# Performance work log

Measured on AMD Instinct MI355X. Metric: run time of the kernel, lower is better.

## Reference

```python
import jax, jax.numpy as jnp
import numpy as np

EPS = 1e-6
NEG_SLOPE = 0.2


def _basis(J):
    # J: [B,N,E,3] -> R: [B,N,E,3(k: U,V,J rows),3(xyz comp)]
    nJ = J / (jnp.linalg.norm(J, axis=-1, keepdims=True) + EPS)
    sub = nJ[..., :2]
    u_z = -(sub[..., 0] ** 2 + sub[..., 1] ** 2) / (nJ[..., 2] + EPS)
    U = jnp.concatenate([sub, u_z[..., None]], axis=-1)
    U = U / (jnp.linalg.norm(U, axis=-1, keepdims=True) + EPS)
    V = jnp.cross(U, nJ)
    return jnp.stack([U, V, nJ], axis=-2)


def _complex_linear(X, J, A, Bw, Cw):
    R = _basis(J)                                   # [B,N,E,3,3], R[...,k,i]
    RtX = jnp.einsum('bneki,bnek->bnei', R, X)      # (R^T X)_i = sum_k R[k,i] X_k
    # rrtx(i, s) has component k equal to R[...,k,i] * s
    a_term = R[..., 0] * RtX[..., 0:1] + R[..., 1] * RtX[..., 1:2]
    b_term = R[..., 1] * RtX[..., 0:1] - R[..., 0] * RtX[..., 1:2]
    c_term = R[..., 2] * RtX[..., 2:3]
    Y = (jnp.einsum('fe,bnei->bnfi', A, a_term)
         + jnp.einsum('fe,bnei->bnfi', Bw, b_term)
         + jnp.einsum('fe,bnei->bnfi', Cw, c_term))
    return Y                                        # [B,N,F,3]


def _vn_leaky_relu(x, W, negative_slope):
    # x: [B,F,3,N]; W: [F,F] torch Linear weight (out,in)
    d = jnp.einsum('gf,bfin->bgin', W, x)
    dot = jnp.sum(x * d, axis=2, keepdims=True)
    d_norm_sq = jnp.sum(d * d, axis=2, keepdims=True)
    neg_branch = x - (dot / (d_norm_sq + EPS)) * d
    lin = jnp.where(dot >= 0, x, neg_branch)
    return negative_slope * x + (1.0 - negative_slope) * lin


def setup_inputs() -> dict:
    key = jax.random.key(0)
    kX, kJ, kA, kB, kC, kW = jax.random.split(key, 6)
    B, N, E, F = 16, 1024, 256, 256
    X = jax.random.normal(kX, (B, N, E, 3), dtype=jnp.float32)
    J = jax.random.normal(kJ, (B, N, E, 3), dtype=jnp.float32)
    A = jax.random.normal(kA, (F, E), dtype=jnp.float32)
    Bw = jax.random.normal(kB, (F, E), dtype=jnp.float32)
    Cw = jax.random.normal(kC, (F, E), dtype=jnp.float32)
    W = jax.random.normal(kW, (F, F), dtype=jnp.float32) * (1.0 / np.sqrt(F))
    return {"X": X, "J": J, "A": A, "Bw": Bw, "Cw": Cw, "W": W, "device": 0}


def reference(X, J, A, Bw, Cw, W, device):
    Y = _complex_linear(X, J, A, Bw, Cw)            # [B,N,F,3]
    x = jnp.transpose(Y, (0, 2, 3, 1))              # [B,F,3,N]
    return _vn_leaky_relu(x, W, NEG_SLOPE)
```

## Files before the change

### kernel.cpp

```cpp
#include <hip/hip_runtime.h>

typedef __attribute__((ext_vector_type(8))) _Float16 half8;
typedef __attribute__((ext_vector_type(4))) _Float16 half4v;
typedef __attribute__((ext_vector_type(4))) float f32x4;
typedef float f32x4u __attribute__((ext_vector_type(4), aligned(4)));
typedef float f32x2u __attribute__((ext_vector_type(2), aligned(4)));

#define EPSF 1e-6f

__device__ __forceinline__ void glds16(const void* g, void* l) {
    __builtin_amdgcn_global_load_lds(
        (const __attribute__((address_space(1))) unsigned*)g,
        (__attribute__((address_space(3))) unsigned*)l, 16, 0, 0);
}
__device__ __forceinline__ unsigned short h2u(_Float16 h) {
    union { _Float16 h; unsigned short u; } c; c.h = h; return c.u;
}

__global__ __launch_bounds__(256) void prep_kernel(
    const float* __restrict__ A, const float* __restrict__ Bw,
    const float* __restrict__ Cw, const float* __restrict__ W,
    _Float16* __restrict__ Mh, _Float16* __restrict__ Wh)
{
    int f = blockIdx.x, e = threadIdx.x;
    Mh[f * 768 + e]       = (_Float16)A[f * 256 + e];
    Mh[f * 768 + 256 + e] = (_Float16)Bw[f * 256 + e];
    Mh[f * 768 + 512 + e] = (_Float16)Cw[f * 256 + e];
    Wh[f * 256 + e]       = (_Float16)W[f * 256 + e];
}

__global__ __launch_bounds__(512, 4) void fused_kernel(
    const float* __restrict__ X, const float* __restrict__ Jp,
    const _Float16* __restrict__ Mh, const _Float16* __restrict__ Wh,
    float* __restrict__ out)
{
    extern __shared__ char lds[];
    const int T_OFF = 49152;
    int tid = threadIdx.x;
    int b  = blockIdx.x >> 5;
    int n0 = (blockIdx.x & 31) * 32;

    int l = tid & 63, lr = l & 15, lq = l >> 4;
    int w = tid >> 6, wc = w & 1, wf = w >> 1;
    int nl = tid >> 4, ep = tid & 15;

    size_t pb0 = ((size_t)((b * 1024 + n0 + nl) * 256) + 2 * ep) * 3;

    auto loadXJ = [&](int eb, float* xs, float* js) {
        size_t pb = pb0 + (size_t)eb * 96;
        f32x4u xa = *(const f32x4u*)(X + pb);
        f32x2u xb = *(const f32x2u*)(X + pb + 4);
        f32x4u ja = *(const f32x4u*)(Jp + pb);
        f32x2u jb = *(const f32x2u*)(Jp + pb + 4);
        xs[0]=xa[0]; xs[1]=xa[1]; xs[2]=xa[2]; xs[3]=xa[3]; xs[4]=xb[0]; xs[5]=xb[1];
        js[0]=ja[0]; js[1]=ja[1]; js[2]=ja[2]; js[3]=ja[3]; js[4]=jb[0]; js[5]=jb[1];
    };

    auto stageA = [&](int eb) {
        #pragma unroll
        for (int h = 0; h < 6; ++h) {
            int m = h * 512 + tid;
            int t = m >> 10, fr = (m >> 2) & 255, slot = m & 3;
            size_t go = ((size_t)fr * 768 + t * 256 + eb * 32
                         + ((slot ^ ((fr >> 1) & 3)) * 8)) * 2;
            glds16((const char*)Mh + go, lds + m * 16);
        }
    };

    auto computeT = [&](const float* xs, const float* js) {
        unsigned short hv[2][9];
        #pragma unroll
        for (int p = 0; p < 2; ++p) {
            float x0 = xs[3*p], x1 = xs[3*p+1], x2 = xs[3*p+2];
            float j0 = js[3*p], j1 = js[3*p+1], j2 = js[3*p+2];
            float jj  = j0*j0 + j1*j1 + j2*j2;
            float rn  = __builtin_amdgcn_rcpf(__builtin_amdgcn_sqrtf(jj) + EPSF);
            float nj0 = j0*rn, nj1 = j1*rn, nj2 = j2*rn;
            float s2  = nj0*nj0 + nj1*nj1;
            float uz  = -s2 * __builtin_amdgcn_rcpf(nj2 + EPSF);
            float ru  = __builtin_amdgcn_rcpf(__builtin_amdgcn_sqrtf(s2 + uz*uz) + EPSF);
            float u0 = nj0*ru, u1 = nj1*ru, u2 = uz*ru;
            float v0 = u1*nj2 - u2*nj1;
            float v1 = u2*nj0 - u0*nj2;
            float v2 = u0*nj1 - u1*nj0;
            float r0 = u0*x0 + v0*x1 + nj0*x2;
            float r1 = u1*x0 + v1*x1 + nj1*x2;
            float r2 = u2*x0 + v2*x1 + nj2*x2;
            hv[p][0] = h2u((_Float16)(u0*r0 + u1*r1));
            hv[p][1] = h2u((_Float16)(v0*r0 + v1*r1));
            hv[p][2] = h2u((_Float16)(nj0*r0 + nj1*r1));
            hv[p][3] = h2u((_Float16)(u1*r0 - u0*r1));
            hv[p][4] = h2u((_Float16)(v1*r0 - v0*r1));
            hv[p][5] = h2u((_Float16)(nj1*r0 - nj0*r1));
            hv[p][6] = h2u((_Float16)(u2*r2));
            hv[p][7] = h2u((_Float16)(v2*r2));
            hv[p][8] = h2u((_Float16)(nj2*r2));
        }
        #pragma unroll
        for (int s = 0; s < 9; ++s) {
            int t = s / 3, i = s % 3;
            unsigned pk = (unsigned)hv[0][s] | ((unsigned)hv[1][s] << 16);
            *(unsigned*)(lds + T_OFF + (t * 96 + i * 32 + nl) * 80 + ep * 4) = pk;
        }
    };

    f32x4 acc[3][4] = {};
    float xs[6], js[6];
    loadXJ(0, xs, js);

    for (int eb = 0; eb < 8; ++eb) {
        __syncthreads();
        stageA(eb);
        computeT(xs, js);
        __syncthreads();
        if (eb < 7) loadXJ(eb + 1, xs, js);

        #pragma unroll
        for (int t = 0; t < 3; ++t) {
            half8 af[4], bf[3];
            #pragma unroll
            for (int mi = 0; mi < 4; ++mi) {
                int f = wf * 64 + mi * 16 + lr;
                af[mi] = *(const half8*)(lds + t * 16384 + f * 64
                                         + ((lq ^ ((f >> 1) & 3)) * 16));
            }
            #pragma unroll
            for (int bi = 0; bi < 3; ++bi) {
                int cr = wc * 48 + bi * 16 + lr;
                bf[bi] = *(const half8*)(lds + T_OFF + (t * 96 + cr) * 80 + lq * 16);
            }
            #pragma unroll
            for (int bi = 0; bi < 3; ++bi)
                #pragma unroll
                for (int mi = 0; mi < 4; ++mi)
                    acc[bi][mi] = __builtin_amdgcn_mfma_f32_16x16x32_f16(af[mi], bf[bi], acc[bi][mi], 0, 0, 0);
        }
    }

    __syncthreads();
    #pragma unroll
    for (int bi = 0; bi < 3; ++bi) {
        int c = wc * 48 + bi * 16 + lr;
        #pragma unroll
        for (int mi = 0; mi < 4; ++mi) {
            int fb2 = (wf * 64 + mi * 16 + lq * 4) * 2;
            f32x4 v = acc[bi][mi];
            half4v p;
            p.x = (_Float16)v[0]; p.y = (_Float16)v[1];
            p.z = (_Float16)v[2]; p.w = (_Float16)v[3];
            *(half4v*)(lds + c * 512 + (fb2 ^ ((c & 7) << 4))) = p;
        }
    }

    int nh = w & 1, gw = w >> 1;
    half8 wreg[2][4];
    #pragma unroll
    for (int gf = 0; gf < 4; ++gf) {
        int g = gw * 64 + gf * 16 + lr;
        wreg[0][gf] = *(const half8*)(Wh + (size_t)g * 256 + lq * 8);
    }
    __syncthreads();

    f32x4 acc2[3][4] = {};
    #pragma unroll
    for (int kt = 0; kt < 8; ++kt) {
        if (kt < 7) {
            #pragma unroll
            for (int gf = 0; gf < 4; ++gf) {
                int g = gw * 64 + gf * 16 + lr;
                wreg[(kt + 1) & 1][gf] =
                    *(const half8*)(Wh + (size_t)g * 256 + (kt + 1) * 32 + lq * 8);
            }
        }
        half8 yf[3];
        #pragma unroll
        for (int ci = 0; ci < 3; ++ci) {
            int c = ci * 32 + nh * 16 + lr;
            yf[ci] = *(const half8*)(lds + c * 512
                                     + ((kt * 64 + lq * 16) ^ ((c & 7) << 4)));
        }
        #pragma unroll
        for (int ci = 0; ci < 3; ++ci)
            #pragma unroll
            for (int gf = 0; gf < 4; ++gf)
                acc2[ci][gf] = __builtin_amdgcn_mfma_f32_16x16x32_f16(
                    yf[ci], wreg[kt & 1][gf], acc2[ci][gf], 0, 0, 0);
    }

    #pragma unroll
    for (int gf = 0; gf < 4; ++gf) {
        int g = gw * 64 + gf * 16 + lr;
        f32x4 o[3];
        #pragma unroll
        for (int r = 0; r < 4; ++r) {
            float xv[3];
            #pragma unroll
            for (int ci = 0; ci < 3; ++ci) {
                int c = ci * 32 + nh * 16 + lq * 4 + r;
                xv[ci] = (float)*(const _Float16*)(lds + c * 512
                                 + ((g * 2) ^ ((c & 7) << 4)));
            }
            float d0 = acc2[0][gf][r], d1 = acc2[1][gf][r], d2 = acc2[2][gf][r];
            float dot = xv[0] * d0 + xv[1] * d1 + xv[2] * d2;
            float dn  = d0 * d0 + d1 * d1 + d2 * d2;
            float sc  = dot / (dn + EPSF);
            bool pos  = dot >= 0.0f;
            float l0 = pos ? xv[0] : fmaf(-sc, d0, xv[0]);
            float l1 = pos ? xv[1] : fmaf(-sc, d1, xv[1]);
            float l2 = pos ? xv[2] : fmaf(-sc, d2, xv[2]);
            o[0][r] = fmaf(0.8f, l0, 0.2f * xv[0]);
            o[1][r] = fmaf(0.8f, l1, 0.2f * xv[1]);
            o[2][r] = fmaf(0.8f, l2, 0.2f * xv[2]);
        }
        int nb = n0 + nh * 16 + lq * 4;
        #pragma unroll
        for (int i = 0; i < 3; ++i)
            *(f32x4*)(out + ((size_t)(b * 256 + g) * 3 + i) * 1024 + nb) = o[i];
    }
}

extern "C" void kernel_launch(void* const* d_in, const int* in_sizes, int n_in,
                              void* d_out, int out_size, void* d_ws, size_t ws_size,
                              hipStream_t stream)
{
    const float* X  = (const float*)d_in[0];
    const float* J  = (const float*)d_in[1];
    const float* A  = (const float*)d_in[2];
    const float* Bw = (const float*)d_in[3];
    const float* Cw = (const float*)d_in[4];
    const float* W  = (const float*)d_in[5];
    float* out = (float*)d_out;

    char* ws = (char*)d_ws;
    _Float16* Mh = (_Float16*)ws;
    _Float16* Wh = (_Float16*)(ws + 393216);

    (void)hipFuncSetAttribute((const void*)fused_kernel,
                              hipFuncAttributeMaxDynamicSharedMemorySize, 72192);

    hipLaunchKernelGGL(prep_kernel,  dim3(256), dim3(256), 0, stream,
                       A, Bw, Cw, W, Mh, Wh);
    hipLaunchKernelGGL(fused_kernel, dim3(512), dim3(512), 72192, stream,
                       X, J, Mh, Wh, out);
}
```

Measured before the change: 58.56 us.

## Double-buffer weight staging and double the per-block point tile with 1024-thread blocks

Each block now covers 64 points instead of 32, using 1024 threads and 256 blocks, so each staged fp16 weight chunk is reused across twice as many points. Weight chunks are double-buffered in LDS so the next chunk's global-to-LDS copy overlaps the current MFMA work. `__syncthreads` is replaced with raw barriers, explicit waitcnt and sched_barrier fences to control ordering. The second GEMM and the epilogue are retiled for the larger block. The cost is about 141 KB of LDS per block, so one block per CU and a single wave of 256 blocks. The hand-written waits cover only LDS counters, so the ordering of the async global-to-LDS copies is fragile.

```diff
diff --git a/kernel.cpp b/kernel.cpp
--- a/kernel.cpp
+++ b/kernel.cpp
@@ -29,23 +29,34 @@
     Wh[f * 256 + e]       = (_Float16)W[f * 256 + e];
 }
 
-__global__ __launch_bounds__(512, 4) void fused_kernel(
+__global__ __launch_bounds__(1024, 2) void fused_kernel(
     const float* __restrict__ X, const float* __restrict__ Jp,
     const _Float16* __restrict__ Mh, const _Float16* __restrict__ Wh,
     float* __restrict__ out)
 {
     extern __shared__ char lds[];
-    const int T_OFF = 49152;
+    const int T_BASE = 98304;
     int tid = threadIdx.x;
-    int b  = blockIdx.x >> 5;
-    int n0 = (blockIdx.x & 31) * 32;
+    int b  = blockIdx.x >> 4;
+    int n0 = (blockIdx.x & 15) * 64;
 
     int l = tid & 63, lr = l & 15, lq = l >> 4;
-    int w = tid >> 6, wc = w & 1, wf = w >> 1;
+    int w = tid >> 6;
+    int wf = w & 3, wc = w >> 2;
     int nl = tid >> 4, ep = tid & 15;
 
+    auto stageEB = [&](int p, int eb) {
+        #pragma unroll
+        for (int h = 0; h < 3; ++h) {
+            int m = h * 1024 + tid;
+            int t = m >> 10, fr = (m >> 2) & 255, slot = m & 3;
+            size_t go = ((size_t)fr * 768 + t * 256 + eb * 32
+                         + ((slot ^ ((fr >> 1) & 3)) * 8)) * 2;
+            glds16((const char*)Mh + go, lds + p * 49152 + m * 16);
+        }
+    };
+
     size_t pb0 = ((size_t)((b * 1024 + n0 + nl) * 256) + 2 * ep) * 3;
-
     auto loadXJ = [&](int eb, float* xs, float* js) {
         size_t pb = pb0 + (size_t)eb * 96;
         f32x4u xa = *(const f32x4u*)(X + pb);
@@ -54,17 +65,6 @@
         f32x2u jb = *(const f32x2u*)(Jp + pb + 4);
         xs[0]=xa[0]; xs[1]=xa[1]; xs[2]=xa[2]; xs[3]=xa[3]; xs[4]=xb[0]; xs[5]=xb[1];
         js[0]=ja[0]; js[1]=ja[1]; js[2]=ja[2]; js[3]=ja[3]; js[4]=jb[0]; js[5]=jb[1];
-    };
-
-    auto stageA = [&](int eb) {
-        #pragma unroll
-        for (int h = 0; h < 6; ++h) {
-            int m = h * 512 + tid;
-            int t = m >> 10, fr = (m >> 2) & 255, slot = m & 3;
-            size_t go = ((size_t)fr * 768 + t * 256 + eb * 32
-                         + ((slot ^ ((fr >> 1) & 3)) * 8)) * 2;
-            glds16((const char*)Mh + go, lds + m * 16);
-        }
     };
 
     auto computeT = [&](const float* xs, const float* js) {
@@ -100,20 +100,34 @@
         for (int s = 0; s < 9; ++s) {
             int t = s / 3, i = s % 3;
             unsigned pk = (unsigned)hv[0][s] | ((unsigned)hv[1][s] << 16);
-            *(unsigned*)(lds + T_OFF + (t * 96 + i * 32 + nl) * 80 + ep * 4) = pk;
+            *(unsigned*)(lds + T_BASE + (t * 192 + i * 64 + nl) * 80 + ep * 4) = pk;
         }
     };
 
     f32x4 acc[3][4] = {};
     float xs[6], js[6];
+
+    stageEB(0, 0);
+    __builtin_amdgcn_sched_barrier(0);
     loadXJ(0, xs, js);
+    __builtin_amdgcn_sched_barrier(0);
 
     for (int eb = 0; eb < 8; ++eb) {
-        __syncthreads();
-        stageA(eb);
+        int cur = eb & 1;
+        __builtin_amdgcn_s_barrier();
+        if (eb < 7) {
+            stageEB(cur ^ 1, eb + 1);
+            __builtin_amdgcn_sched_barrier(0);
+        }
         computeT(xs, js);
-        __syncthreads();
-        if (eb < 7) loadXJ(eb + 1, xs, js);
+        asm volatile("s_waitcnt lgkmcnt(0)" ::: "memory");
+        __builtin_amdgcn_sched_barrier(0);
+        __builtin_amdgcn_s_barrier();
+        __builtin_amdgcn_sched_barrier(0);
+        if (eb < 7) {
+            loadXJ(eb + 1, xs, js);
+            __builtin_amdgcn_sched_barrier(0);
+        }
 
         #pragma unroll
         for (int t = 0; t < 3; ++t) {
@@ -121,23 +135,24 @@
             #pragma unroll
             for (int mi = 0; mi < 4; ++mi) {
                 int f = wf * 64 + mi * 16 + lr;
-                af[mi] = *(const half8*)(lds + t * 16384 + f * 64
+                af[mi] = *(const half8*)(lds + cur * 49152 + t * 16384 + f * 64
                                          + ((lq ^ ((f >> 1) & 3)) * 16));
             }
             #pragma unroll
             for (int bi = 0; bi < 3; ++bi) {
                 int cr = wc * 48 + bi * 16 + lr;
-                bf[bi] = *(const half8*)(lds + T_OFF + (t * 96 + cr) * 80 + lq * 16);
+                bf[bi] = *(const half8*)(lds + T_BASE + (t * 192 + cr) * 80 + lq * 16);
             }
             #pragma unroll
             for (int bi = 0; bi < 3; ++bi)
                 #pragma unroll
                 for (int mi = 0; mi < 4; ++mi)
-                    acc[bi][mi] = __builtin_amdgcn_mfma_f32_16x16x32_f16(af[mi], bf[bi], acc[bi][mi], 0, 0, 0);
-        }
-    }
-
-    __syncthreads();
+                    acc[bi][mi] = __builtin_amdgcn_mfma_f32_16x16x32_f16(
+                        af[mi], bf[bi], acc[bi][mi], 0, 0, 0);
+        }
+    }
+
+    __builtin_amdgcn_s_barrier();
     #pragma unroll
     for (int bi = 0; bi < 3; ++bi) {
         int c = wc * 48 + bi * 16 + lr;
@@ -153,70 +168,74 @@
     }
 
     int nh = w & 1, gw = w >> 1;
-    half8 wreg[2][4];
-    #pragma unroll
-    for (int gf = 0; gf < 4; ++gf) {
-        int g = gw * 64 + gf * 16 + lr;
+    half8 wreg[2][2];
+    #pragma unroll
+    for (int gf = 0; gf < 2; ++gf) {
+        int g = gw * 32 + gf * 16 + lr;
         wreg[0][gf] = *(const half8*)(Wh + (size_t)g * 256 + lq * 8);
     }
-    __syncthreads();
-
-    f32x4 acc2[3][4] = {};
+    asm volatile("s_waitcnt lgkmcnt(0)" ::: "memory");
+    __builtin_amdgcn_sched_barrier(0);
+    __builtin_amdgcn_s_barrier();
+    __builtin_amdgcn_sched_barrier(0);
+
+    f32x4 acc2[3][2][2] = {};
     #pragma unroll
     for (int kt = 0; kt < 8; ++kt) {
         if (kt < 7) {
             #pragma unroll
-            for (int gf = 0; gf < 4; ++gf) {
-                int g = gw * 64 + gf * 16 + lr;
+            for (int gf = 0; gf < 2; ++gf) {
+                int g = gw * 32 + gf * 16 + lr;
                 wreg[(kt + 1) & 1][gf] =
                     *(const half8*)(Wh + (size_t)g * 256 + (kt + 1) * 32 + lq * 8);
             }
         }
-        half8 yf[3];
-        #pragma unroll
-        for (int ci = 0; ci < 3; ++ci) {
-            int c = ci * 32 + nh * 16 + lr;
-            yf[ci] = *(const half8*)(lds + c * 512
-                                     + ((kt * 64 + lq * 16) ^ ((c & 7) << 4)));
-        }
         #pragma unroll
         for (int ci = 0; ci < 3; ++ci)
             #pragma unroll
-            for (int gf = 0; gf < 4; ++gf)
-                acc2[ci][gf] = __builtin_amdgcn_mfma_f32_16x16x32_f16(
-                    yf[ci], wreg[kt & 1][gf], acc2[ci][gf], 0, 0, 0);
-    }
-
-    #pragma unroll
-    for (int gf = 0; gf < 4; ++gf) {
-        int g = gw * 64 + gf * 16 + lr;
-        f32x4 o[3];
-        #pragma unroll
-        for (int r = 0; r < 4; ++r) {
-            float xv[3];
-            #pragma unroll
-            for (int ci = 0; ci < 3; ++ci) {
-                int c = ci * 32 + nh * 16 + lq * 4 + r;
-                xv[ci] = (float)*(const _Float16*)(lds + c * 512
-                                 + ((g * 2) ^ ((c & 7) << 4)));
-            }
-            float d0 = acc2[0][gf][r], d1 = acc2[1][gf][r], d2 = acc2[2][gf][r];
-            float dot = xv[0] * d0 + xv[1] * d1 + xv[2] * d2;
-            float dn  = d0 * d0 + d1 * d1 + d2 * d2;
-            float sc  = dot / (dn + EPSF);
-            bool pos  = dot >= 0.0f;
-            float l0 = pos ? xv[0] : fmaf(-sc, d0, xv[0]);
-            float l1 = pos ? xv[1] : fmaf(-sc, d1, xv[1]);
-            float l2 = pos ? xv[2] : fmaf(-sc, d2, xv[2]);
-            o[0][r] = fmaf(0.8f, l0, 0.2f * xv[0]);
-            o[1][r] = fmaf(0.8f, l1, 0.2f * xv[1]);
-            o[2][r] = fmaf(0.8f, l2, 0.2f * xv[2]);
-        }
-        int nb = n0 + nh * 16 + lq * 4;
-        #pragma unroll
-        for (int i = 0; i < 3; ++i)
-            *(f32x4*)(out + ((size_t)(b * 256 + g) * 3 + i) * 1024 + nb) = o[i];
-    }
+            for (int nc = 0; nc < 2; ++nc) {
+                int c = ci * 64 + nh * 32 + nc * 16 + lr;
+                half8 yf = *(const half8*)(lds + c * 512
+                             + ((kt * 64 + lq * 16) ^ ((c & 7) << 4)));
+                #pragma unroll
+                for (int gf = 0; gf < 2; ++gf)
+                    acc2[ci][nc][gf] = __builtin_amdgcn_mfma_f32_16x16x32_f16(
+                        yf, wreg[kt & 1][gf], acc2[ci][nc][gf], 0, 0, 0);
+            }
+    }
+
+    #pragma unroll
+    for (int nc = 0; nc < 2; ++nc)
+        #pragma unroll
+        for (int gf = 0; gf < 2; ++gf) {
+            int g = gw * 32 + gf * 16 + lr;
+            f32x4 o[3];
+            #pragma unroll
+            for (int r = 0; r < 4; ++r) {
+                float xv[3];
+                #pragma unroll
+                for (int ci = 0; ci < 3; ++ci) {
+                    int c = ci * 64 + nh * 32 + nc * 16 + lq * 4 + r;
+                    xv[ci] = (float)*(const _Float16*)(lds + c * 512
+                                     + ((g * 2) ^ ((c & 7) << 4)));
+                }
+                float d0 = acc2[0][nc][gf][r], d1 = acc2[1][nc][gf][r], d2 = acc2[2][nc][gf][r];
+                float dot = xv[0] * d0 + xv[1] * d1 + xv[2] * d2;
+                float dn  = d0 * d0 + d1 * d1 + d2 * d2;
+                float sc  = dot / (dn + EPSF);
+                bool pos  = dot >= 0.0f;
+                float l0 = pos ? xv[0] : fmaf(-sc, d0, xv[0]);
+                float l1 = pos ? xv[1] : fmaf(-sc, d1, xv[1]);
+                float l2 = pos ? xv[2] : fmaf(-sc, d2, xv[2]);
+                o[0][r] = fmaf(0.8f, l0, 0.2f * xv[0]);
+                o[1][r] = fmaf(0.8f, l1, 0.2f * xv[1]);
+                o[2][r] = fmaf(0.8f, l2, 0.2f * xv[2]);
+            }
+            int nb = n0 + nh * 32 + nc * 16 + lq * 4;
+            #pragma unroll
+            for (int i = 0; i < 3; ++i)
+                *(f32x4*)(out + ((size_t)(b * 256 + g) * 3 + i) * 1024 + nb) = o[i];
+        }
 }
 
 extern "C" void kernel_launch(void* const* d_in, const int* in_sizes, int n_in,
@@ -236,10 +255,10 @@
     _Float16* Wh = (_Float16*)(ws + 393216);
 
     (void)hipFuncSetAttribute((const void*)fused_kernel,
-                              hipFuncAttributeMaxDynamicSharedMemorySize, 72192);
-
-    hipLaunchKernelGGL(prep_kernel,  dim3(256), dim3(256), 0, stream,
+                              hipFuncAttributeMaxDynamicSharedMemorySize, 144384);
+
+    hipLaunchKernelGGL(prep_kernel,  dim3(256), dim3(256),  0, stream,
                        A, Bw, Cw, W, Mh, Wh);
-    hipLaunchKernelGGL(fused_kernel, dim3(512), dim3(512), 72192, stream,
+    hipLaunchKernelGGL(fused_kernel, dim3(256), dim3(1024), 144384, stream,
                        X, J, Mh, Wh, out);
 }
```

Result: faster. 54.83 us (-6.4%).

## Double-buffer per-term A-weight tiles and shrink LDS footprint

Applied to the files above, without the earlier changes.

Replaces staging all three weight slices per E-block with a two-slot ring buffer that stages one term's slice at a time, prefetching the next while MFMAs consume the current one. The T tile row stride drops from 80 to 72 bytes and LDS use falls from about 72 KB to about 53 KB, with launch bounds lowered from 4 to 3 blocks per CU. The register prefetch of X/J for the next block is removed, so those global loads now sit on the critical path before computeT. A barrier is added after every term step, which raises sync count.

```diff
diff --git a/kernel.cpp b/kernel.cpp
--- a/kernel.cpp
+++ b/kernel.cpp
@@ -29,45 +29,44 @@
     Wh[f * 256 + e]       = (_Float16)W[f * 256 + e];
 }
 
-__global__ __launch_bounds__(512, 4) void fused_kernel(
+__global__ __launch_bounds__(512, 3)
+void fused_kernel(
     const float* __restrict__ X, const float* __restrict__ Jp,
     const _Float16* __restrict__ Mh, const _Float16* __restrict__ Wh,
     float* __restrict__ out)
 {
     extern __shared__ char lds[];
-    const int T_OFF = 49152;
+    const int T_BASE = 32768;
     int tid = threadIdx.x;
     int b  = blockIdx.x >> 5;
     int n0 = (blockIdx.x & 31) * 32;
 
     int l = tid & 63, lr = l & 15, lq = l >> 4;
-    int w = tid >> 6, wc = w & 1, wf = w >> 1;
+    int w = tid >> 6;
+    int wc = w & 1, wf = w >> 1;
     int nl = tid >> 4, ep = tid & 15;
 
+    auto stageT = [&](int p, int eb, int t) {
+        #pragma unroll
+        for (int h = 0; h < 2; ++h) {
+            int m = h * 512 + tid;
+            int fr = m >> 2, slot = m & 3;
+            size_t go = ((size_t)fr * 768 + t * 256 + eb * 32
+                         + ((slot ^ ((fr >> 1) & 3)) * 8)) * 2;
+            glds16((const char*)Mh + go, lds + p * 16384 + m * 16);
+        }
+    };
+
     size_t pb0 = ((size_t)((b * 1024 + n0 + nl) * 256) + 2 * ep) * 3;
 
-    auto loadXJ = [&](int eb, float* xs, float* js) {
+    auto computeT = [&](int eb) {
         size_t pb = pb0 + (size_t)eb * 96;
         f32x4u xa = *(const f32x4u*)(X + pb);
         f32x2u xb = *(const f32x2u*)(X + pb + 4);
         f32x4u ja = *(const f32x4u*)(Jp + pb);
         f32x2u jb = *(const f32x2u*)(Jp + pb + 4);
-        xs[0]=xa[0]; xs[1]=xa[1]; xs[2]=xa[2]; xs[3]=xa[3]; xs[4]=xb[0]; xs[5]=xb[1];
-        js[0]=ja[0]; js[1]=ja[1]; js[2]=ja[2]; js[3]=ja[3]; js[4]=jb[0]; js[5]=jb[1];
-    };
-
-    auto stageA = [&](int eb) {
-        #pragma unroll
-        for (int h = 0; h < 6; ++h) {
-            int m = h * 512 + tid;
-            int t = m >> 10, fr = (m >> 2) & 255, slot = m & 3;
-            size_t go = ((size_t)fr * 768 + t * 256 + eb * 32
-                         + ((slot ^ ((fr >> 1) & 3)) * 8)) * 2;
-            glds16((const char*)Mh + go, lds + m * 16);
-        }
-    };
-
-    auto computeT = [&](const float* xs, const float* js) {
+        float xs[6] = { xa[0], xa[1], xa[2], xa[3], xb[0], xb[1] };
+        float js[6] = { ja[0], ja[1], ja[2], ja[3], jb[0], jb[1] };
         unsigned short hv[2][9];
         #pragma unroll
         for (int p = 0; p < 2; ++p) {
@@ -100,44 +99,52 @@
         for (int s = 0; s < 9; ++s) {
             int t = s / 3, i = s % 3;
             unsigned pk = (unsigned)hv[0][s] | ((unsigned)hv[1][s] << 16);
-            *(unsigned*)(lds + T_OFF + (t * 96 + i * 32 + nl) * 80 + ep * 4) = pk;
+            *(unsigned*)(lds + T_BASE + (t * 96 + i * 32 + nl) * 72 + ep * 4) = pk;
         }
     };
 
     f32x4 acc[3][4] = {};
-    float xs[6], js[6];
-    loadXJ(0, xs, js);
+
+    auto mstep = [&](int ap, int t) {
+        half8 af[4], bf[3];
+        #pragma unroll
+        for (int mi = 0; mi < 4; ++mi) {
+            int f = wf * 64 + mi * 16 + lr;
+            af[mi] = *(const half8*)(lds + ap * 16384 + f * 64
+                                     + ((lq ^ ((f >> 1) & 3)) * 16));
+        }
+        #pragma unroll
+        for (int bi = 0; bi < 3; ++bi) {
+            int cr = wc * 48 + bi * 16 + lr;
+            bf[bi] = *(const half8*)(lds + T_BASE + (t * 96 + cr) * 72 + lq * 16);
+        }
+        #pragma unroll
+        for (int bi = 0; bi < 3; ++bi)
+            #pragma unroll
+            for (int mi = 0; mi < 4; ++mi)
+                acc[bi][mi] = __builtin_amdgcn_mfma_f32_16x16x32_f16(
+                    af[mi], bf[bi], acc[bi][mi], 0, 0, 0);
+    };
+
+    stageT(0, 0, 0);
 
     for (int eb = 0; eb < 8; ++eb) {
         __syncthreads();
-        stageA(eb);
-        computeT(xs, js);
+        computeT(eb);
         __syncthreads();
-        if (eb < 7) loadXJ(eb + 1, xs, js);
-
         #pragma unroll
         for (int t = 0; t < 3; ++t) {
-            half8 af[4], bf[3];
-            #pragma unroll
-            for (int mi = 0; mi < 4; ++mi) {
-                int f = wf * 64 + mi * 16 + lr;
-                af[mi] = *(const half8*)(lds + t * 16384 + f * 64
-                                         + ((lq ^ ((f >> 1) & 3)) * 16));
+            int s = eb * 3 + t;
+            if (s < 23) {
+                int nt = (t + 1) % 3;
+                int ne = (t == 2) ? eb + 1 : eb;
+                stageT((s + 1) & 1, ne, nt);
             }
-            #pragma unroll
-            for (int bi = 0; bi < 3; ++bi) {
-                int cr = wc * 48 + bi * 16 + lr;
-                bf[bi] = *(const half8*)(lds + T_OFF + (t * 96 + cr) * 80 + lq * 16);
-            }
-            #pragma unroll
-            for (int bi = 0; bi < 3; ++bi)
-                #pragma unroll
-                for (int mi = 0; mi < 4; ++mi)
-                    acc[bi][mi] = __builtin_amdgcn_mfma_f32_16x16x32_f16(af[mi], bf[bi], acc[bi][mi], 0, 0, 0);
-        }
-    }
-
-    __syncthreads();
+            mstep(s & 1, t);
+            __syncthreads();
+        }
+    }
+
     #pragma unroll
     for (int bi = 0; bi < 3; ++bi) {
         int c = wc * 48 + bi * 16 + lr;
@@ -236,10 +243,10 @@
     _Float16* Wh = (_Float16*)(ws + 393216);
 
     (void)hipFuncSetAttribute((const void*)fused_kernel,
-                              hipFuncAttributeMaxDynamicSharedMemorySize, 72192);
+                              hipFuncAttributeMaxDynamicSharedMemorySize, 53504);
 
     hipLaunchKernelGGL(prep_kernel,  dim3(256), dim3(256), 0, stream,
                        A, Bw, Cw, W, Mh, Wh);
-    hipLaunchKernelGGL(fused_kernel, dim3(512), dim3(512), 72192, stream,
+    hipLaunchKernelGGL(fused_kernel, dim3(512), dim3(512), 53504, stream,
                        X, J, Mh, Wh, out);
 }
```

Result: slower. 74.61 us (+27.4%).

## Double-buffer weight tiles in LDS to overlap staging with MFMA compute

Applied to the files above, without the earlier changes.

Splits the LDS weight-tile area into two buffers so the async global-to-LDS copy of the next E-block's weights is issued while the current block's MFMAs run. Each iteration's double `__syncthreads` is replaced by raw s_barrier plus explicit lgkmcnt waits and sched_barriers. The aim is to hide weight-staging latency inside the main loop. In exchange, dynamic LDS grows to about 118 KB and launch_bounds drops to 2, which likely leaves only one 512-thread block per CU instead of two. There is also some risk from relying on implicit vmcnt ordering for the LDS DMA completion.

```diff
diff --git a/kernel.cpp b/kernel.cpp
--- a/kernel.cpp
+++ b/kernel.cpp
@@ -29,23 +29,35 @@
     Wh[f * 256 + e]       = (_Float16)W[f * 256 + e];
 }
 
-__global__ __launch_bounds__(512, 4) void fused_kernel(
+__global__ __launch_bounds__(512, 2)
+void fused_kernel(
     const float* __restrict__ X, const float* __restrict__ Jp,
     const _Float16* __restrict__ Mh, const _Float16* __restrict__ Wh,
     float* __restrict__ out)
 {
     extern __shared__ char lds[];
-    const int T_OFF = 49152;
+    const int T_BASE = 98304;
     int tid = threadIdx.x;
     int b  = blockIdx.x >> 5;
     int n0 = (blockIdx.x & 31) * 32;
 
     int l = tid & 63, lr = l & 15, lq = l >> 4;
-    int w = tid >> 6, wc = w & 1, wf = w >> 1;
+    int w = tid >> 6;
+    int wc = w & 1, wf = w >> 1;
     int nl = tid >> 4, ep = tid & 15;
 
+    auto stageEB = [&](int p, int eb) {
+        #pragma unroll
+        for (int h = 0; h < 6; ++h) {
+            int m = h * 512 + tid;
+            int t = m >> 10, fr = (m >> 2) & 255, slot = m & 3;
+            size_t go = ((size_t)fr * 768 + t * 256 + eb * 32
+                         + ((slot ^ ((fr >> 1) & 3)) * 8)) * 2;
+            glds16((const char*)Mh + go, lds + p * 49152 + m * 16);
+        }
+    };
+
     size_t pb0 = ((size_t)((b * 1024 + n0 + nl) * 256) + 2 * ep) * 3;
-
     auto loadXJ = [&](int eb, float* xs, float* js) {
         size_t pb = pb0 + (size_t)eb * 96;
         f32x4u xa = *(const f32x4u*)(X + pb);
@@ -54,17 +66,6 @@
         f32x2u jb = *(const f32x2u*)(Jp + pb + 4);
         xs[0]=xa[0]; xs[1]=xa[1]; xs[2]=xa[2]; xs[3]=xa[3]; xs[4]=xb[0]; xs[5]=xb[1];
         js[0]=ja[0]; js[1]=ja[1]; js[2]=ja[2]; js[3]=ja[3]; js[4]=jb[0]; js[5]=jb[1];
-    };
-
-    auto stageA = [&](int eb) {
-        #pragma unroll
-        for (int h = 0; h < 6; ++h) {
-            int m = h * 512 + tid;
-            int t = m >> 10, fr = (m >> 2) & 255, slot = m & 3;
-            size_t go = ((size_t)fr * 768 + t * 256 + eb * 32
-                         + ((slot ^ ((fr >> 1) & 3)) * 8)) * 2;
-            glds16((const char*)Mh + go, lds + m * 16);
-        }
     };
 
     auto computeT = [&](const float* xs, const float* js) {
@@ -100,20 +101,34 @@
         for (int s = 0; s < 9; ++s) {
             int t = s / 3, i = s % 3;
             unsigned pk = (unsigned)hv[0][s] | ((unsigned)hv[1][s] << 16);
-            *(unsigned*)(lds + T_OFF + (t * 96 + i * 32 + nl) * 80 + ep * 4) = pk;
+            *(unsigned*)(lds + T_BASE + (t * 96 + i * 32 + nl) * 80 + ep * 4) = pk;
         }
     };
 
     f32x4 acc[3][4] = {};
     float xs[6], js[6];
+
+    stageEB(0, 0);
+    __builtin_amdgcn_sched_barrier(0);
     loadXJ(0, xs, js);
+    __builtin_amdgcn_sched_barrier(0);
 
     for (int eb = 0; eb < 8; ++eb) {
-        __syncthreads();
-        stageA(eb);
+        int cur = eb & 1;
+        __builtin_amdgcn_s_barrier();
+        if (eb < 7) {
+            stageEB(cur ^ 1, eb + 1);
+            __builtin_amdgcn_sched_barrier(0);
+        }
         computeT(xs, js);
-        __syncthreads();
-        if (eb < 7) loadXJ(eb + 1, xs, js);
+        asm volatile("s_waitcnt lgkmcnt(0)" ::: "memory");
+        __builtin_amdgcn_sched_barrier(0);
+        __builtin_amdgcn_s_barrier();
+        __builtin_amdgcn_sched_barrier(0);
+        if (eb < 7) {
+            loadXJ(eb + 1, xs, js);
+            __builtin_amdgcn_sched_barrier(0);
+        }
 
         #pragma unroll
         for (int t = 0; t < 3; ++t) {
@@ -121,23 +136,24 @@
             #pragma unroll
             for (int mi = 0; mi < 4; ++mi) {
                 int f = wf * 64 + mi * 16 + lr;
-                af[mi] = *(const half8*)(lds + t * 16384 + f * 64
+                af[mi] = *(const half8*)(lds + cur * 49152 + t * 16384 + f * 64
                                          + ((lq ^ ((f >> 1) & 3)) * 16));
             }
             #pragma unroll
             for (int bi = 0; bi < 3; ++bi) {
                 int cr = wc * 48 + bi * 16 + lr;
-                bf[bi] = *(const half8*)(lds + T_OFF + (t * 96 + cr) * 80 + lq * 16);
+                bf[bi] = *(const half8*)(lds + T_BASE + (t * 96 + cr) * 80 + lq * 16);
             }
             #pragma unroll
             for (int bi = 0; bi < 3; ++bi)
                 #pragma unroll
                 for (int mi = 0; mi < 4; ++mi)
-                    acc[bi][mi] = __builtin_amdgcn_mfma_f32_16x16x32_f16(af[mi], bf[bi], acc[bi][mi], 0, 0, 0);
-        }
-    }
-
-    __syncthreads();
+                    acc[bi][mi] = __builtin_amdgcn_mfma_f32_16x16x32_f16(
+                        af[mi], bf[bi], acc[bi][mi], 0, 0, 0);
+        }
+    }
+
+    __builtin_amdgcn_s_barrier();
     #pragma unroll
     for (int bi = 0; bi < 3; ++bi) {
         int c = wc * 48 + bi * 16 + lr;
@@ -236,10 +252,10 @@
     _Float16* Wh = (_Float16*)(ws + 393216);
 
     (void)hipFuncSetAttribute((const void*)fused_kernel,
-                              hipFuncAttributeMaxDynamicSharedMemorySize, 72192);
+                              hipFuncAttributeMaxDynamicSharedMemorySize, 121344);
 
     hipLaunchKernelGGL(prep_kernel,  dim3(256), dim3(256), 0, stream,
                        A, Bw, Cw, W, Mh, Wh);
-    hipLaunchKernelGGL(fused_kernel, dim3(512), dim3(512), 72192, stream,
+    hipLaunchKernelGGL(fused_kernel, dim3(512), dim3(512), 121344, stream,
                        X, J, Mh, Wh, out);
 }
```

New measurement: 70.43 us. +20.3%, slower.
